# Kernel optimization log

Hardware: AMD Instinct MI355X
Metric: run time of the kernel (lower is better)

Reference implementation:

```python
import jax, jax.numpy as jnp
import numpy as np

N_NODES = 100000
N_EDGES = 1250000
D_FEAT = 64


def setup_inputs() -> dict:
    key = jax.random.key(0)
    k1, k2 = jax.random.split(key)
    x = jax.random.normal(k1, (N_NODES, D_FEAT), dtype=jnp.float32)
    edge_index = jax.random.randint(k2, (2, N_EDGES), 0, N_NODES, dtype=jnp.int64)
    return {"t": 0, "x": x, "edge_index": edge_index}


def reference(t, x, edge_index):
    # LGConv(normalize=False): out[i] = sum_{(j->i) in E} x[j]
    # adj_t SpMM expressed as gather + segment-sum scatter.
    src = edge_index[0]  # source/neighbor nodes
    dst = edge_index[1]  # destination nodes
    msgs = x[src]  # [E, D] gather
    out = jax.ops.segment_sum(msgs, dst, num_segments=N_NODES)  # [N, D]
    return out
```

## Files before the change

kernel.cpp:

```cpp
#include <hip/hip_runtime.h>

#define N_NODES 100000
#define N_EDGES 1250000
#define D_FEAT 64

#define NB_SHIFT 7
#define NODES_PER_B 128
#define N_BUCKETS ((N_NODES + NODES_PER_B - 1) / NODES_PER_B)
#define TROW (N_BUCKETS + 1)
#define NB_PAD 1024
#define MAX_BUCKET_EDGES 2048
#define SRC_BITS 17
#define SRC_MASK ((1u << SRC_BITS) - 1u)

__global__ __launch_bounds__(256) void lgconv_scatter(
    const float* __restrict__ x, const int* __restrict__ src,
    const int* __restrict__ dst, float* __restrict__ out) {
    int tid  = blockIdx.x * blockDim.x + threadIdx.x;
    int edge = tid >> 4;
    int f4   = (tid & 15) << 2;
    if (edge >= N_EDGES) return;
    int s = src[edge], d = dst[edge];
    const float4 v = *reinterpret_cast<const float4*>(x + (size_t)s * D_FEAT + f4);
    float* o = out + (size_t)d * D_FEAT + f4;
    unsafeAtomicAdd(o + 0, v.x); unsafeAtomicAdd(o + 1, v.y);
    unsafeAtomicAdd(o + 2, v.z); unsafeAtomicAdd(o + 3, v.w);
}

template <int CHUNK, int BLOCK>
__global__ __launch_bounds__(BLOCK) void k1_sort(
    const int* __restrict__ src, const int* __restrict__ dst,
    unsigned int* __restrict__ bins, int* __restrict__ table) {
    __shared__ int hist[NB_PAD];
    __shared__ int scanBase[NB_PAD];
    __shared__ int cur[NB_PAD];
    __shared__ int scanTmp[BLOCK];
    __shared__ unsigned int stage[CHUNK];
    const int t    = threadIdx.x;
    const int c    = blockIdx.x;
    const int base = c * CHUNK;
    const int cnt  = min(CHUNK, N_EDGES - base);
    for (int i = t; i < NB_PAD; i += BLOCK) { hist[i] = 0; cur[i] = 0; }
    __syncthreads();
    for (int i = t; i < cnt; i += BLOCK)
        atomicAdd(&hist[dst[base + i] >> NB_SHIFT], 1);
    __syncthreads();
    constexpr int P = NB_PAD / BLOCK;
    int loc[P]; int tsum = 0;
    #pragma unroll
    for (int q = 0; q < P; ++q) { loc[q] = hist[t * P + q]; tsum += loc[q]; }
    scanTmp[t] = tsum;
    __syncthreads();
    for (int off = 1; off < BLOCK; off <<= 1) {
        int u = (t >= off) ? scanTmp[t - off] : 0;
        __syncthreads();
        scanTmp[t] += u;
        __syncthreads();
    }
    int run = scanTmp[t] - tsum;
    #pragma unroll
    for (int q = 0; q < P; ++q) { scanBase[t * P + q] = run; run += loc[q]; }
    __syncthreads();
    for (int i = t; i < TROW; i += BLOCK) table[c * TROW + i] = scanBase[i];
    for (int i = t; i < cnt; i += BLOCK) {
        int d = dst[base + i], s = src[base + i];
        int b = d >> NB_SHIFT;
        unsigned int packed = ((unsigned int)(d & (NODES_PER_B - 1)) << SRC_BITS)
                            | (unsigned int)s;
        int pos = scanBase[b] + atomicAdd(&cur[b], 1);
        stage[pos] = packed;
    }
    __syncthreads();
    for (int i = t; i < cnt; i += BLOCK) bins[base + i] = stage[i];
}

template <int CHUNK, int NCH>
__global__ __launch_bounds__(256) void k2_accum(
    const float* __restrict__ x, const unsigned int* __restrict__ bins,
    const int* __restrict__ table, float* __restrict__ out) {
    constexpr int CPT = (NCH + 255) / 256;
    constexpr int LPC = CHUNK / 256;
    constexpr int CPI = 256 / LPC;
    __shared__ int            startA[CPT * 256];
    __shared__ unsigned short lenA[CPT * 256];
    __shared__ int            destB[CPT * 256];
    __shared__ int            scanTmp[256];
    __shared__ unsigned int   raw[MAX_BUCKET_EDGES];
    __shared__ unsigned int   srcs[MAX_BUCKET_EDGES];
    __shared__ int cntArr[NODES_PER_B];
    __shared__ int nodeOff[NODES_PER_B + 1];
    __shared__ int curN[NODES_PER_B];
    __shared__ int s2[NODES_PER_B];
    const int t = threadIdx.x;
    const int b = blockIdx.x;

    int myLen[CPT]; int lsum = 0;
    #pragma unroll
    for (int q = 0; q < CPT; ++q) {
        int c = t * CPT + q;
        int st = 0, len = 0;
        if (c < NCH) {
            st  = table[c * TROW + b];
            len = table[c * TROW + b + 1] - st;
        }
        startA[t * CPT + q] = st;
        lenA[t * CPT + q]   = (unsigned short)len;
        myLen[q] = len; lsum += len;
    }
    scanTmp[t] = lsum;
    __syncthreads();
    for (int off = 1; off < 256; off <<= 1) {
        int u = (t >= off) ? scanTmp[t - off] : 0;
        __syncthreads();
        scanTmp[t] += u;
        __syncthreads();
    }
    int run = scanTmp[t] - lsum;
    #pragma unroll
    for (int q = 0; q < CPT; ++q) { destB[t * CPT + q] = run; run += myLen[q]; }
    int cntTot = scanTmp[255];
    if (cntTot > MAX_BUCKET_EDGES) cntTot = MAX_BUCKET_EDGES;
    __syncthreads();

    const int cj = t / LPC;
    const int jj = t % LPC;
    for (int c0 = 0; c0 < NCH; c0 += CPI) {
        int c = c0 + cj;
        if (c < NCH) {
            int len = lenA[c], st = startA[c], db = destB[c];
            const unsigned int* p = bins + (size_t)c * CHUNK + st;
            if (jj < len) raw[db + jj] = p[jj];
            if (jj == LPC - 1)
                for (int q = LPC; q < len; ++q) raw[db + q] = p[q];
        }
    }
    __syncthreads();

    if (t < NODES_PER_B) cntArr[t] = 0;
    __syncthreads();
    for (int i = t; i < cntTot; i += 256)
        atomicAdd(&cntArr[raw[i] >> SRC_BITS], 1);
    __syncthreads();
    int v = (t < NODES_PER_B) ? cntArr[t] : 0;
    if (t < NODES_PER_B) s2[t] = v;
    __syncthreads();
    for (int off = 1; off < NODES_PER_B; off <<= 1) {
        int u = (t < NODES_PER_B && t >= off) ? s2[t - off] : 0;
        __syncthreads();
        if (t < NODES_PER_B) s2[t] += u;
        __syncthreads();
    }
    if (t < NODES_PER_B) { nodeOff[t] = s2[t] - v; curN[t] = s2[t] - v; }
    if (t == 0) nodeOff[NODES_PER_B] = cntTot;
    __syncthreads();
    for (int i = t; i < cntTot; i += 256) {
        unsigned int p = raw[i];
        int pos = atomicAdd(&curN[p >> SRC_BITS], 1);
        srcs[pos] = p & SRC_MASK;
    }
    __syncthreads();

    int lane4 = (t & 15) << 2;
    for (int g = 0; g < NODES_PER_B / 16; ++g) {
        int local = g * 16 + (t >> 4);
        int node  = b * NODES_PER_B + local;
        int beg = nodeOff[local], end = nodeOff[local + 1];
        float4 acc = make_float4(0.f, 0.f, 0.f, 0.f);
        int k = beg;
        for (; k + 3 < end; k += 4) {
            unsigned int i0 = srcs[k], i1 = srcs[k+1], i2 = srcs[k+2], i3 = srcs[k+3];
            const float4 a = *reinterpret_cast<const float4*>(x + (size_t)i0 * D_FEAT + lane4);
            const float4 c = *reinterpret_cast<const float4*>(x + (size_t)i1 * D_FEAT + lane4);
            const float4 d = *reinterpret_cast<const float4*>(x + (size_t)i2 * D_FEAT + lane4);
            const float4 e = *reinterpret_cast<const float4*>(x + (size_t)i3 * D_FEAT + lane4);
            acc.x += a.x + c.x + d.x + e.x;
            acc.y += a.y + c.y + d.y + e.y;
            acc.z += a.z + c.z + d.z + e.z;
            acc.w += a.w + c.w + d.w + e.w;
        }
        for (; k < end; ++k) {
            unsigned int i0 = srcs[k];
            const float4 a = *reinterpret_cast<const float4*>(x + (size_t)i0 * D_FEAT + lane4);
            acc.x += a.x; acc.y += a.y; acc.z += a.z; acc.w += a.w;
        }
        if (node < N_NODES)
            *reinterpret_cast<float4*>(out + (size_t)node * D_FEAT + lane4) = acc;
    }
}

extern "C" void kernel_launch(void* const* d_in, const int* in_sizes, int n_in,
                              void* d_out, int out_size, void* d_ws, size_t ws_size,
                              hipStream_t stream) {
    const float* x   = (const float*)d_in[1];
    const int*   ei  = (const int*)d_in[2];
    const int*   src = ei;
    const int*   dst = ei + N_EDGES;
    float*       out = (float*)d_out;

    constexpr int CH1  = 2048;
    constexpr int NCH1 = (N_EDGES + CH1 - 1) / CH1;
    constexpr int CH2  = 4096;
    constexpr int NCH2 = (N_EDGES + CH2 - 1) / CH2;
    const size_t need1 = ((size_t)N_EDGES + (size_t)NCH1 * TROW) * sizeof(int);
    const size_t need2 = ((size_t)N_EDGES + (size_t)NCH2 * TROW) * sizeof(int);

    if (ws_size >= need1) {
        unsigned int* bins  = (unsigned int*)d_ws;
        int*          table = (int*)(bins + N_EDGES);
        k1_sort<CH1, 256><<<NCH1, 256, 0, stream>>>(src, dst, bins, table);
        k2_accum<CH1, NCH1><<<N_BUCKETS, 256, 0, stream>>>(x, bins, table, out);
    } else if (ws_size >= need2) {
        unsigned int* bins  = (unsigned int*)d_ws;
        int*          table = (int*)(bins + N_EDGES);
        k1_sort<CH2, 512><<<NCH2, 512, 0, stream>>>(src, dst, bins, table);
        k2_accum<CH2, NCH2><<<N_BUCKETS, 256, 0, stream>>>(x, bins, table, out);
    } else {
        hipMemsetAsync(out, 0, (size_t)out_size * sizeof(float), stream);
        const int total = N_EDGES * 16;
        lgconv_scatter<<<(total + 255) / 256, 256, 0, stream>>>(x, src, dst, out);
    }
}
```

Before: 143.2 us.

## Transpose bucket offset table and use 512-thread blocks for sort and accumulate

Adds a tiled transpose kernel so each accumulate block reads its per-chunk start offsets contiguously instead of with a stride of TROW. The chunk-to-thread mapping becomes interleaved to match the coalesced reads. Both the sort and accumulate kernels now run with 512 threads, so each block processes more nodes per gather pass. The cost is an extra kernel launch, a second copy of the table in workspace, and larger per-block shared memory and thread count, which may lower occupancy.

```diff
diff --git a/kernel.cpp b/kernel.cpp
--- a/kernel.cpp
+++ b/kernel.cpp
@@ -74,17 +74,32 @@
     for (int i = t; i < cnt; i += BLOCK) bins[base + i] = stage[i];
 }
 
-template <int CHUNK, int NCH>
-__global__ __launch_bounds__(256) void k2_accum(
+template <int NCH>
+__global__ __launch_bounds__(1024) void t_transpose(
+    const int* __restrict__ table, int* __restrict__ tableT) {
+    __shared__ int tile[32][33];
+    const int tx = threadIdx.x & 31, ty = threadIdx.x >> 5;
+    const int c0 = blockIdx.x * 32;
+    const int b0 = blockIdx.y * 32;
+    int c = c0 + ty, b = b0 + tx;
+    if (c < NCH && b < TROW) tile[ty][tx] = table[c * TROW + b];
+    __syncthreads();
+    b = b0 + ty; c = c0 + tx;
+    if (b < TROW && c < NCH) tableT[b * NCH + c] = tile[tx][ty];
+}
+
+template <int CHUNK, int NCH, int BLOCK, bool USE_T>
+__global__ __launch_bounds__(BLOCK) void k2_accum(
     const float* __restrict__ x, const unsigned int* __restrict__ bins,
-    const int* __restrict__ table, float* __restrict__ out) {
-    constexpr int CPT = (NCH + 255) / 256;
-    constexpr int LPC = CHUNK / 256;
-    constexpr int CPI = 256 / LPC;
-    __shared__ int            startA[CPT * 256];
-    __shared__ unsigned short lenA[CPT * 256];
-    __shared__ int            destB[CPT * 256];
-    __shared__ int            scanTmp[256];
+    const int* __restrict__ tab, float* __restrict__ out) {
+    constexpr int CPT  = (NCH + BLOCK - 1) / BLOCK;
+    constexpr int NCHP = CPT * BLOCK;
+    constexpr int LPC  = CHUNK / BLOCK;
+    constexpr int CPI  = BLOCK / LPC;
+    __shared__ int            startA[NCHP];
+    __shared__ unsigned short lenA[NCHP];
+    __shared__ int            destB[NCHP];
+    __shared__ int            scanTmp[BLOCK];
     __shared__ unsigned int   raw[MAX_BUCKET_EDGES];
     __shared__ unsigned int   srcs[MAX_BUCKET_EDGES];
     __shared__ int cntArr[NODES_PER_B];
@@ -94,22 +109,27 @@
     const int t = threadIdx.x;
     const int b = blockIdx.x;
 
-    int myLen[CPT]; int lsum = 0;
+    int ln[CPT]; int lsum = 0;
     #pragma unroll
     for (int q = 0; q < CPT; ++q) {
-        int c = t * CPT + q;
+        int c = q * BLOCK + t;
         int st = 0, len = 0;
         if (c < NCH) {
-            st  = table[c * TROW + b];
-            len = table[c * TROW + b + 1] - st;
-        }
-        startA[t * CPT + q] = st;
-        lenA[t * CPT + q]   = (unsigned short)len;
-        myLen[q] = len; lsum += len;
+            if (USE_T) {
+                st  = tab[b * NCH + c];
+                len = tab[(b + 1) * NCH + c] - st;
+            } else {
+                st  = tab[c * TROW + b];
+                len = tab[c * TROW + b + 1] - st;
+            }
+        }
+        startA[c < NCHP ? c : 0] = st;
+        lenA[c < NCHP ? c : 0]   = (unsigned short)len;
+        ln[q] = len; lsum += len;
     }
     scanTmp[t] = lsum;
     __syncthreads();
-    for (int off = 1; off < 256; off <<= 1) {
+    for (int off = 1; off < BLOCK; off <<= 1) {
         int u = (t >= off) ? scanTmp[t - off] : 0;
         __syncthreads();
         scanTmp[t] += u;
@@ -117,8 +137,8 @@
     }
     int run = scanTmp[t] - lsum;
     #pragma unroll
-    for (int q = 0; q < CPT; ++q) { destB[t * CPT + q] = run; run += myLen[q]; }
-    int cntTot = scanTmp[255];
+    for (int q = 0; q < CPT; ++q) { destB[q * BLOCK + t] = run; run += ln[q]; }
+    int cntTot = scanTmp[BLOCK - 1];
     if (cntTot > MAX_BUCKET_EDGES) cntTot = MAX_BUCKET_EDGES;
     __syncthreads();
 
@@ -138,7 +158,7 @@
 
     if (t < NODES_PER_B) cntArr[t] = 0;
     __syncthreads();
-    for (int i = t; i < cntTot; i += 256)
+    for (int i = t; i < cntTot; i += BLOCK)
         atomicAdd(&cntArr[raw[i] >> SRC_BITS], 1);
     __syncthreads();
     int v = (t < NODES_PER_B) ? cntArr[t] : 0;
@@ -153,7 +173,7 @@
     if (t < NODES_PER_B) { nodeOff[t] = s2[t] - v; curN[t] = s2[t] - v; }
     if (t == 0) nodeOff[NODES_PER_B] = cntTot;
     __syncthreads();
-    for (int i = t; i < cntTot; i += 256) {
+    for (int i = t; i < cntTot; i += BLOCK) {
         unsigned int p = raw[i];
         int pos = atomicAdd(&curN[p >> SRC_BITS], 1);
         srcs[pos] = p & SRC_MASK;
@@ -161,8 +181,9 @@
     __syncthreads();
 
     int lane4 = (t & 15) << 2;
-    for (int g = 0; g < NODES_PER_B / 16; ++g) {
-        int local = g * 16 + (t >> 4);
+    constexpr int NPG = BLOCK / 16;
+    for (int g = 0; g < NODES_PER_B / NPG; ++g) {
+        int local = g * NPG + (t >> 4);
         int node  = b * NODES_PER_B + local;
         int beg = nodeOff[local], end = nodeOff[local + 1];
         float4 acc = make_float4(0.f, 0.f, 0.f, 0.f);
@@ -197,23 +218,24 @@
     const int*   dst = ei + N_EDGES;
     float*       out = (float*)d_out;
 
-    constexpr int CH1  = 2048;
-    constexpr int NCH1 = (N_EDGES + CH1 - 1) / CH1;
-    constexpr int CH2  = 4096;
-    constexpr int NCH2 = (N_EDGES + CH2 - 1) / CH2;
-    const size_t need1 = ((size_t)N_EDGES + (size_t)NCH1 * TROW) * sizeof(int);
-    const size_t need2 = ((size_t)N_EDGES + (size_t)NCH2 * TROW) * sizeof(int);
-
-    if (ws_size >= need1) {
+    constexpr int CH   = 2048;
+    constexpr int NCHV = (N_EDGES + CH - 1) / CH;
+    const size_t need_full = ((size_t)N_EDGES + 2 * (size_t)NCHV * TROW) * sizeof(int);
+    const size_t need_r4   = ((size_t)N_EDGES +     (size_t)NCHV * TROW) * sizeof(int);
+
+    if (ws_size >= need_full) {
+        unsigned int* bins   = (unsigned int*)d_ws;
+        int*          table  = (int*)(bins + N_EDGES);
+        int*          tableT = table + (size_t)NCHV * TROW;
+        k1_sort<CH, 512><<<NCHV, 512, 0, stream>>>(src, dst, bins, table);
+        dim3 tg((NCHV + 31) / 32, (TROW + 31) / 32);
+        t_transpose<NCHV><<<tg, 1024, 0, stream>>>(table, tableT);
+        k2_accum<CH, NCHV, 512, true><<<N_BUCKETS, 512, 0, stream>>>(x, bins, tableT, out);
+    } else if (ws_size >= need_r4) {
         unsigned int* bins  = (unsigned int*)d_ws;
         int*          table = (int*)(bins + N_EDGES);
-        k1_sort<CH1, 256><<<NCH1, 256, 0, stream>>>(src, dst, bins, table);
-        k2_accum<CH1, NCH1><<<N_BUCKETS, 256, 0, stream>>>(x, bins, table, out);
-    } else if (ws_size >= need2) {
-        unsigned int* bins  = (unsigned int*)d_ws;
-        int*          table = (int*)(bins + N_EDGES);
-        k1_sort<CH2, 512><<<NCH2, 512, 0, stream>>>(src, dst, bins, table);
-        k2_accum<CH2, NCH2><<<N_BUCKETS, 256, 0, stream>>>(x, bins, table, out);
+        k1_sort<CH, 512><<<NCHV, 512, 0, stream>>>(src, dst, bins, table);
+        k2_accum<CH, NCHV, 512, false><<<N_BUCKETS, 512, 0, stream>>>(x, bins, table, out);
     } else {
         hipMemsetAsync(out, 0, (size_t)out_size * sizeof(float), stream);
         const int total = N_EDGES * 16;
```

New measurement: 144.8 us. No clear change (+1.1%).

## Sort bucket edges by source slice for gather locality, enlarge chunks and blocks

Applied to the files above, without the earlier changes.

The first pass now sorts 8192-edge chunks with 1024-thread blocks, which cuts the number of chunks and the size of the chunk table. The second pass uses 512 threads and counting-sorts each bucket's edges by (source-id slice, destination node) instead of by destination alone. Each node's neighbours are then visited slice by slice, so concurrent blocks tend to gather from similar source regions of x and share L2. The cost is 13 segment loops per node with shorter unrolling, larger shared memory per block, and a wider scan.

```diff
diff --git a/kernel.cpp b/kernel.cpp
--- a/kernel.cpp
+++ b/kernel.cpp
@@ -12,6 +12,13 @@
 #define MAX_BUCKET_EDGES 2048
 #define SRC_BITS 17
 #define SRC_MASK ((1u << SRC_BITS) - 1u)
+
+#define CH 8192
+#define NCH ((N_EDGES + CH - 1) / CH)
+#define SL_SHIFT 13
+#define N_SLICES 13
+#define KEYS (N_SLICES * NODES_PER_B)
+#define KPAD 2048
 
 __global__ __launch_bounds__(256) void lgconv_scatter(
     const float* __restrict__ x, const int* __restrict__ src,
@@ -27,42 +34,36 @@
     unsafeAtomicAdd(o + 2, v.z); unsafeAtomicAdd(o + 3, v.w);
 }
 
-template <int CHUNK, int BLOCK>
-__global__ __launch_bounds__(BLOCK) void k1_sort(
+__global__ __launch_bounds__(1024) void k1_sort(
     const int* __restrict__ src, const int* __restrict__ dst,
     unsigned int* __restrict__ bins, int* __restrict__ table) {
     __shared__ int hist[NB_PAD];
     __shared__ int scanBase[NB_PAD];
     __shared__ int cur[NB_PAD];
-    __shared__ int scanTmp[BLOCK];
-    __shared__ unsigned int stage[CHUNK];
+    __shared__ int scanTmp[1024];
+    __shared__ unsigned int stage[CH];
     const int t    = threadIdx.x;
     const int c    = blockIdx.x;
-    const int base = c * CHUNK;
-    const int cnt  = min(CHUNK, N_EDGES - base);
-    for (int i = t; i < NB_PAD; i += BLOCK) { hist[i] = 0; cur[i] = 0; }
-    __syncthreads();
-    for (int i = t; i < cnt; i += BLOCK)
+    const int base = c * CH;
+    const int cnt  = min(CH, N_EDGES - base);
+    hist[t] = 0; cur[t] = 0;
+    __syncthreads();
+    for (int i = t; i < cnt; i += 1024)
         atomicAdd(&hist[dst[base + i] >> NB_SHIFT], 1);
     __syncthreads();
-    constexpr int P = NB_PAD / BLOCK;
-    int loc[P]; int tsum = 0;
-    #pragma unroll
-    for (int q = 0; q < P; ++q) { loc[q] = hist[t * P + q]; tsum += loc[q]; }
-    scanTmp[t] = tsum;
-    __syncthreads();
-    for (int off = 1; off < BLOCK; off <<= 1) {
+    int v = hist[t];
+    scanTmp[t] = v;
+    __syncthreads();
+    for (int off = 1; off < 1024; off <<= 1) {
         int u = (t >= off) ? scanTmp[t - off] : 0;
         __syncthreads();
         scanTmp[t] += u;
         __syncthreads();
     }
-    int run = scanTmp[t] - tsum;
-    #pragma unroll
-    for (int q = 0; q < P; ++q) { scanBase[t * P + q] = run; run += loc[q]; }
-    __syncthreads();
-    for (int i = t; i < TROW; i += BLOCK) table[c * TROW + i] = scanBase[i];
-    for (int i = t; i < cnt; i += BLOCK) {
+    scanBase[t] = scanTmp[t] - v;
+    __syncthreads();
+    if (t < TROW) table[c * TROW + t] = scanBase[t];
+    for (int i = t; i < cnt; i += 1024) {
         int d = dst[base + i], s = src[base + i];
         int b = d >> NB_SHIFT;
         unsigned int packed = ((unsigned int)(d & (NODES_PER_B - 1)) << SRC_BITS)
@@ -71,117 +72,117 @@
         stage[pos] = packed;
     }
     __syncthreads();
-    for (int i = t; i < cnt; i += BLOCK) bins[base + i] = stage[i];
-}
-
-template <int CHUNK, int NCH>
-__global__ __launch_bounds__(256) void k2_accum(
+    for (int i = t; i < cnt; i += 1024) bins[base + i] = stage[i];
+}
+
+__global__ __launch_bounds__(512) void k2_accum(
     const float* __restrict__ x, const unsigned int* __restrict__ bins,
     const int* __restrict__ table, float* __restrict__ out) {
-    constexpr int CPT = (NCH + 255) / 256;
-    constexpr int LPC = CHUNK / 256;
-    constexpr int CPI = 256 / LPC;
-    __shared__ int            startA[CPT * 256];
-    __shared__ unsigned short lenA[CPT * 256];
-    __shared__ int            destB[CPT * 256];
-    __shared__ int            scanTmp[256];
+    __shared__ int            startA[512];
+    __shared__ unsigned short lenA[512];
+    __shared__ int            destB[512];
+    __shared__ int            scanTmp[512];
     __shared__ unsigned int   raw[MAX_BUCKET_EDGES];
     __shared__ unsigned int   srcs[MAX_BUCKET_EDGES];
-    __shared__ int cntArr[NODES_PER_B];
-    __shared__ int nodeOff[NODES_PER_B + 1];
-    __shared__ int curN[NODES_PER_B];
-    __shared__ int s2[NODES_PER_B];
+    __shared__ int            cnt2[KPAD];
+    __shared__ int            off2[KPAD];
+    __shared__ int            cur2[KPAD];
     const int t = threadIdx.x;
     const int b = blockIdx.x;
 
-    int myLen[CPT]; int lsum = 0;
+    int st = 0, len = 0;
+    if (t < NCH) {
+        st  = table[t * TROW + b];
+        len = table[t * TROW + b + 1] - st;
+    }
+    startA[t] = st;
+    lenA[t]   = (unsigned short)len;
+    scanTmp[t] = len;
+    __syncthreads();
+    for (int off = 1; off < 512; off <<= 1) {
+        int u = (t >= off) ? scanTmp[t - off] : 0;
+        __syncthreads();
+        scanTmp[t] += u;
+        __syncthreads();
+    }
+    destB[t] = scanTmp[t] - len;
+    int cntTot = scanTmp[511];
+    if (cntTot > MAX_BUCKET_EDGES) cntTot = MAX_BUCKET_EDGES;
     #pragma unroll
-    for (int q = 0; q < CPT; ++q) {
-        int c = t * CPT + q;
-        int st = 0, len = 0;
-        if (c < NCH) {
-            st  = table[c * TROW + b];
-            len = table[c * TROW + b + 1] - st;
+    for (int q = 0; q < KPAD / 512; ++q) cnt2[q * 512 + t] = 0;
+    __syncthreads();
+
+    {
+        const int cj = t >> 4;
+        const int jj = t & 15;
+        for (int c0 = 0; c0 < NCH; c0 += 32) {
+            int c = c0 + cj;
+            if (c < NCH) {
+                int l = lenA[c], s0 = startA[c], db = destB[c];
+                const unsigned int* p = bins + (size_t)c * CH + s0;
+                if (jj < l) raw[db + jj] = p[jj];
+                if (jj == 15)
+                    for (int q = 16; q < l; ++q) raw[db + q] = p[q];
+            }
         }
-        startA[t * CPT + q] = st;
-        lenA[t * CPT + q]   = (unsigned short)len;
-        myLen[q] = len; lsum += len;
-    }
-    scanTmp[t] = lsum;
-    __syncthreads();
-    for (int off = 1; off < 256; off <<= 1) {
-        int u = (t >= off) ? scanTmp[t - off] : 0;
-        __syncthreads();
-        scanTmp[t] += u;
-        __syncthreads();
-    }
-    int run = scanTmp[t] - lsum;
-    #pragma unroll
-    for (int q = 0; q < CPT; ++q) { destB[t * CPT + q] = run; run += myLen[q]; }
-    int cntTot = scanTmp[255];
-    if (cntTot > MAX_BUCKET_EDGES) cntTot = MAX_BUCKET_EDGES;
-    __syncthreads();
-
-    const int cj = t / LPC;
-    const int jj = t % LPC;
-    for (int c0 = 0; c0 < NCH; c0 += CPI) {
-        int c = c0 + cj;
-        if (c < NCH) {
-            int len = lenA[c], st = startA[c], db = destB[c];
-            const unsigned int* p = bins + (size_t)c * CHUNK + st;
-            if (jj < len) raw[db + jj] = p[jj];
-            if (jj == LPC - 1)
-                for (int q = LPC; q < len; ++q) raw[db + q] = p[q];
+    }
+    __syncthreads();
+
+    for (int i = t; i < cntTot; i += 512) {
+        unsigned int p = raw[i];
+        int key = (int)(((p & SRC_MASK) >> SL_SHIFT) << NB_SHIFT) | (int)(p >> SRC_BITS);
+        atomicAdd(&cnt2[key], 1);
+    }
+    __syncthreads();
+    {
+        int l0 = cnt2[4 * t], l1 = cnt2[4 * t + 1], l2 = cnt2[4 * t + 2], l3 = cnt2[4 * t + 3];
+        int tsum = l0 + l1 + l2 + l3;
+        scanTmp[t] = tsum;
+        __syncthreads();
+        for (int off = 1; off < 512; off <<= 1) {
+            int u = (t >= off) ? scanTmp[t - off] : 0;
+            __syncthreads();
+            scanTmp[t] += u;
+            __syncthreads();
         }
-    }
-    __syncthreads();
-
-    if (t < NODES_PER_B) cntArr[t] = 0;
-    __syncthreads();
-    for (int i = t; i < cntTot; i += 256)
-        atomicAdd(&cntArr[raw[i] >> SRC_BITS], 1);
-    __syncthreads();
-    int v = (t < NODES_PER_B) ? cntArr[t] : 0;
-    if (t < NODES_PER_B) s2[t] = v;
-    __syncthreads();
-    for (int off = 1; off < NODES_PER_B; off <<= 1) {
-        int u = (t < NODES_PER_B && t >= off) ? s2[t - off] : 0;
-        __syncthreads();
-        if (t < NODES_PER_B) s2[t] += u;
-        __syncthreads();
-    }
-    if (t < NODES_PER_B) { nodeOff[t] = s2[t] - v; curN[t] = s2[t] - v; }
-    if (t == 0) nodeOff[NODES_PER_B] = cntTot;
-    __syncthreads();
-    for (int i = t; i < cntTot; i += 256) {
+        int run = scanTmp[t] - tsum;
+        off2[4 * t] = run; cur2[4 * t] = run; run += l0;
+        off2[4 * t + 1] = run; cur2[4 * t + 1] = run; run += l1;
+        off2[4 * t + 2] = run; cur2[4 * t + 2] = run; run += l2;
+        off2[4 * t + 3] = run; cur2[4 * t + 3] = run;
+    }
+    __syncthreads();
+    for (int i = t; i < cntTot; i += 512) {
         unsigned int p = raw[i];
-        int pos = atomicAdd(&curN[p >> SRC_BITS], 1);
-        srcs[pos] = p & SRC_MASK;
+        unsigned int s = p & SRC_MASK;
+        int key = (int)((s >> SL_SHIFT) << NB_SHIFT) | (int)(p >> SRC_BITS);
+        int pos = atomicAdd(&cur2[key], 1);
+        srcs[pos] = s;
     }
     __syncthreads();
 
     int lane4 = (t & 15) << 2;
-    for (int g = 0; g < NODES_PER_B / 16; ++g) {
-        int local = g * 16 + (t >> 4);
+    for (int g = 0; g < NODES_PER_B / 32; ++g) {
+        int local = g * 32 + (t >> 4);
         int node  = b * NODES_PER_B + local;
-        int beg = nodeOff[local], end = nodeOff[local + 1];
         float4 acc = make_float4(0.f, 0.f, 0.f, 0.f);
-        int k = beg;
-        for (; k + 3 < end; k += 4) {
-            unsigned int i0 = srcs[k], i1 = srcs[k+1], i2 = srcs[k+2], i3 = srcs[k+3];
-            const float4 a = *reinterpret_cast<const float4*>(x + (size_t)i0 * D_FEAT + lane4);
-            const float4 c = *reinterpret_cast<const float4*>(x + (size_t)i1 * D_FEAT + lane4);
-            const float4 d = *reinterpret_cast<const float4*>(x + (size_t)i2 * D_FEAT + lane4);
-            const float4 e = *reinterpret_cast<const float4*>(x + (size_t)i3 * D_FEAT + lane4);
-            acc.x += a.x + c.x + d.x + e.x;
-            acc.y += a.y + c.y + d.y + e.y;
-            acc.z += a.z + c.z + d.z + e.z;
-            acc.w += a.w + c.w + d.w + e.w;
-        }
-        for (; k < end; ++k) {
-            unsigned int i0 = srcs[k];
-            const float4 a = *reinterpret_cast<const float4*>(x + (size_t)i0 * D_FEAT + lane4);
-            acc.x += a.x; acc.y += a.y; acc.z += a.z; acc.w += a.w;
+        #pragma unroll
+        for (int s = 0; s < N_SLICES; ++s) {
+            int idx = (s << NB_SHIFT) + local;
+            int beg = off2[idx], end = off2[idx + 1];
+            int k = beg;
+            for (; k + 1 < end; k += 2) {
+                unsigned int i0 = srcs[k], i1 = srcs[k + 1];
+                const float4 a = *reinterpret_cast<const float4*>(x + (size_t)i0 * D_FEAT + lane4);
+                const float4 c = *reinterpret_cast<const float4*>(x + (size_t)i1 * D_FEAT + lane4);
+                acc.x += a.x + c.x; acc.y += a.y + c.y;
+                acc.z += a.z + c.z; acc.w += a.w + c.w;
+            }
+            if (k < end) {
+                unsigned int i0 = srcs[k];
+                const float4 a = *reinterpret_cast<const float4*>(x + (size_t)i0 * D_FEAT + lane4);
+                acc.x += a.x; acc.y += a.y; acc.z += a.z; acc.w += a.w;
+            }
         }
         if (node < N_NODES)
             *reinterpret_cast<float4*>(out + (size_t)node * D_FEAT + lane4) = acc;
@@ -197,23 +198,13 @@
     const int*   dst = ei + N_EDGES;
     float*       out = (float*)d_out;
 
-    constexpr int CH1  = 2048;
-    constexpr int NCH1 = (N_EDGES + CH1 - 1) / CH1;
-    constexpr int CH2  = 4096;
-    constexpr int NCH2 = (N_EDGES + CH2 - 1) / CH2;
-    const size_t need1 = ((size_t)N_EDGES + (size_t)NCH1 * TROW) * sizeof(int);
-    const size_t need2 = ((size_t)N_EDGES + (size_t)NCH2 * TROW) * sizeof(int);
-
-    if (ws_size >= need1) {
+    const size_t need = ((size_t)N_EDGES + (size_t)NCH * TROW) * sizeof(int);
+
+    if (ws_size >= need) {
         unsigned int* bins  = (unsigned int*)d_ws;
         int*          table = (int*)(bins + N_EDGES);
-        k1_sort<CH1, 256><<<NCH1, 256, 0, stream>>>(src, dst, bins, table);
-        k2_accum<CH1, NCH1><<<N_BUCKETS, 256, 0, stream>>>(x, bins, table, out);
-    } else if (ws_size >= need2) {
-        unsigned int* bins  = (unsigned int*)d_ws;
-        int*          table = (int*)(bins + N_EDGES);
-        k1_sort<CH2, 512><<<NCH2, 512, 0, stream>>>(src, dst, bins, table);
-        k2_accum<CH2, NCH2><<<N_BUCKETS, 256, 0, stream>>>(x, bins, table, out);
+        k1_sort<<<NCH, 1024, 0, stream>>>(src, dst, bins, table);
+        k2_accum<<<N_BUCKETS, 512, 0, stream>>>(x, bins, table, out);
     } else {
         hipMemsetAsync(out, 0, (size_t)out_size * sizeof(float), stream);
         const int total = N_EDGES * 16;
```

Result: slower. 173.5 us (+21.2%).
